# Optimization experiments

Hardware: AMD Instinct MI355X
Metric: run time of the kernel (lower is better)

## Reference

```python
import jax, jax.numpy as jnp
import numpy as np

B, N, Q, D = 1, 6, 10000, 256
HEADS, LEVELS, NPTS, ZANCH = 8, 1, 8, 4  # NPTS = 2*n_points, ZANCH = num_points_in_pillar
HF, WF = 32, 88
HD = D // HEADS


def setup_inputs() -> dict:
    key = jax.random.key(0)
    ks = jax.random.split(key, 18)
    s = 1.0 / np.sqrt(D)
    inp = {
        'queries': jax.random.normal(ks[0], (B, N, Q, D), jnp.float32),
        'pos_emb': jax.random.normal(ks[1], (B, N, Q, D), jnp.float32),
        'lvl_emb': jax.random.normal(ks[2], (LEVELS, D), jnp.float32),
        'cam_emb': jax.random.normal(ks[3], (N, D), jnp.float32),
        'features0': jax.random.normal(ks[4], (B * N, D, HF, WF), jnp.float32),
        'reference_points_3D': jax.random.uniform(ks[5], (B, N, Q, ZANCH, 2), jnp.float32),
        'bev_mask': jax.random.randint(ks[6], (B, N, Q, ZANCH, 2), 0, 2).astype(bool),
        # MSDeformAttn3D params
        'W_value': jax.random.normal(ks[7], (D, D), jnp.float32) * s,
        'b_value': jnp.zeros((D,), jnp.float32),
        'W_off': jax.random.normal(ks[8], (HEADS * LEVELS * NPTS * 2, D), jnp.float32) * 0.01,
        'b_off': jax.random.uniform(ks[9], (HEADS * LEVELS * NPTS * 2,), jnp.float32, -2.0, 2.0),
        'W_attn': jax.random.normal(ks[10], (HEADS * LEVELS * NPTS, D), jnp.float32) * s,
        'b_attn': jnp.zeros((HEADS * LEVELS * NPTS,), jnp.float32),
        'W_inner': jax.random.normal(ks[11], (D, D), jnp.float32) * s,
        'b_inner': jnp.zeros((D,), jnp.float32),
        # SpatialCrossAttention.output_proj
        'W_out': jax.random.normal(ks[12], (D, D), jnp.float32) * s,
        'b_out': jnp.zeros((D,), jnp.float32),
    }
    return inp


def _bilinear(value_t, loc, H, W):
    # value_t: (bn, heads, H*W, hd); loc: (bn, q, heads, pts, 2) normalized to [0,1]
    bn, q, heads, pts, _ = loc.shape
    hd = value_t.shape[-1]
    # grid_sample(2*loc-1, align_corners=False) -> pixel coord = loc*size - 0.5
    x = loc[..., 0] * W - 0.5
    y = loc[..., 1] * H - 0.5
    x0 = jnp.floor(x); y0 = jnp.floor(y)
    dx = x - x0; dy = y - y0
    x0 = x0.astype(jnp.int32); y0 = y0.astype(jnp.int32)
    out = jnp.zeros((bn, heads, q * pts, hd), value_t.dtype)
    corners = ((0, 0, (1 - dx) * (1 - dy)), (1, 0, dx * (1 - dy)),
               (0, 1, (1 - dx) * dy), (1, 1, dx * dy))
    for ox, oy, w in corners:
        xi = x0 + ox; yi = y0 + oy
        valid = (xi >= 0) & (xi < W) & (yi >= 0) & (yi < H)  # zero padding
        wgt = jnp.where(valid, w, 0.0)
        idx = jnp.clip(yi, 0, H - 1) * W + jnp.clip(xi, 0, W - 1)  # (bn,q,heads,pts)
        idx_t = idx.transpose(0, 2, 1, 3).reshape(bn, heads, q * pts)
        g = jnp.take_along_axis(value_t, idx_t[..., None], axis=2)  # (bn,heads,q*pts,hd)
        wgt_t = wgt.transpose(0, 2, 1, 3).reshape(bn, heads, q * pts)
        out = out + g * wgt_t[..., None]
    return out.reshape(bn, heads, q, pts, hd)


def _forward(queries, pos_emb, lvl_emb, cam_emb, features0, reference_points_3D, bev_mask,
             W_value, b_value, W_off, b_off, W_attn, b_attn, W_inner, b_inner, W_out, b_out):
    b, n, q, d = queries.shape
    hf, wf = features0.shape[-2:]
    # flatten features + level/cam embeddings -> (b*n, hw, d)
    feat = features0.reshape(b, n, d, hf * wf)
    feat = feat + lvl_emb[0][None, None, :, None] + cam_emb[None, :, :, None]
    input_flatten = feat.transpose(0, 1, 3, 2).reshape(b * n, hf * wf, d)

    qp = (queries + pos_emb).reshape(b * n, q, d)
    ref = reference_points_3D.reshape(b * n, q, ZANCH, 2)

    # --- MSDeformAttn3D (single level) ---
    value = (input_flatten @ W_value.T + b_value).reshape(b * n, hf * wf, HEADS, HD)
    off = (qp @ W_off.T + b_off).reshape(b * n, q, HEADS, LEVELS, NPTS, 2)
    attw = jax.nn.softmax((qp @ W_attn.T + b_attn).reshape(b * n, q, HEADS, LEVELS * NPTS), axis=-1)
    attw = attw.reshape(b * n, q, HEADS, LEVELS, NPTS)
    normalizer = jnp.array([wf, hf], queries.dtype)  # (W, H)
    pts_per_z = NPTS // ZANCH
    off_z = off.reshape(b * n, q, HEADS, LEVELS, pts_per_z, ZANCH, 2)
    loc = ref[:, :, None, None, None, :, :] + off_z / normalizer
    loc = loc.reshape(b * n, q, HEADS, LEVELS, NPTS, 2)

    value_t = value.transpose(0, 2, 1, 3)  # (bn, heads, hw, hd)
    sampled = _bilinear(value_t, loc[:, :, :, 0], hf, wf)  # (bn,heads,q,pts,hd)
    attw_t = attw[:, :, :, 0].transpose(0, 2, 1, 3)  # (bn,heads,q,pts)
    out = jnp.einsum('bhqp,bhqpc->bqhc', attw_t, sampled).reshape(b * n, q, d)
    out = out @ W_inner.T + b_inner

    # --- scatter back per camera, normalize by hit count ---
    attn = out.reshape(b, n, q, d)
    # indexes come from batch 0's mask (as in the original code)
    hit = (bev_mask[0, :, :, :, 0].astype(jnp.int32).sum(-1) > 0).astype(queries.dtype)  # (n,q)
    slots = (attn * hit[None, :, :, None]).sum(1)  # (b,q,d)
    count = (bev_mask[..., 0].astype(jnp.int32).sum(-1) > 0).astype(queries.dtype).sum(1)
    count = jnp.clip(count, 1.0, None)  # (b,q)
    slots = slots / count[..., None]
    return slots @ W_out.T + b_out


def reference(queries, pos_emb, lvl_emb, cam_emb, features0, reference_points_3D, bev_mask,
              W_value, b_value, W_off, b_off, W_attn, b_attn, W_inner, b_inner, W_out, b_out):
    return _forward(queries, pos_emb, lvl_emb, cam_emb, features0, reference_points_3D, bev_mask,
                    W_value, b_value, W_off, b_off, W_attn, b_attn, W_inner, b_inner, W_out, b_out)
```

## Files before the change

kernel.cpp:

```cpp
#include <hip/hip_runtime.h>
#include <hip/hip_bf16.h>

#define BN     6
#define NQ     10000
#define DIM    256
#define HEADS  8
#define HDD    32
#define HF_    32
#define WF_    88
#define HW_    (HF_*WF_)
#define MTOT   (BN*NQ)

typedef __attribute__((ext_vector_type(8))) unsigned short ushort8_t;
typedef __attribute__((ext_vector_type(8))) short bf16x8;
typedef __attribute__((ext_vector_type(4))) float f32x4;

static __device__ inline unsigned short f2bf(float x) {
    __hip_bfloat16 b = __float2bfloat16(x);
    return *(unsigned short*)&b;
}

__global__ __launch_bounds__(256)
void k_wcvt(const float* __restrict__ Wv, const float* __restrict__ Wo,
            const float* __restrict__ Wa, const float* __restrict__ Wi,
            const float* __restrict__ Wz,
            unsigned short* __restrict__ Wv_bf, unsigned short* __restrict__ Woa_bf,
            unsigned short* __restrict__ Wi_bf, unsigned short* __restrict__ Wz_bf)
{
    const int i4 = (blockIdx.x*256 + threadIdx.x) * 4;
    if (i4 < 65536) {
        float4 v;
        ushort4 p;
        v = *(const float4*)(Wv+i4); p.x=f2bf(v.x);p.y=f2bf(v.y);p.z=f2bf(v.z);p.w=f2bf(v.w);
        *(ushort4*)(Wv_bf+i4) = p;
        v = *(const float4*)(Wi+i4); p.x=f2bf(v.x);p.y=f2bf(v.y);p.z=f2bf(v.z);p.w=f2bf(v.w);
        *(ushort4*)(Wi_bf+i4) = p;
        v = *(const float4*)(Wz+i4); p.x=f2bf(v.x);p.y=f2bf(v.y);p.z=f2bf(v.z);p.w=f2bf(v.w);
        *(ushort4*)(Wz_bf+i4) = p;
    }
    if (i4 < 32768) {
        float4 v = *(const float4*)(Wo+i4);
        ushort4 p; p.x=f2bf(v.x);p.y=f2bf(v.y);p.z=f2bf(v.z);p.w=f2bf(v.w);
        *(ushort4*)(Woa_bf+i4) = p;
    }
    if (i4 < 16384) {
        float4 v = *(const float4*)(Wa+i4);
        ushort4 p; p.x=f2bf(v.x);p.y=f2bf(v.y);p.z=f2bf(v.z);p.w=f2bf(v.w);
        *(ushort4*)(Woa_bf+32768+i4) = p;
    }
}

__global__ __launch_bounds__(256)
void k_ebias(const float* __restrict__ lvl, const float* __restrict__ cam,
             const float* __restrict__ Wv, const float* __restrict__ bv,
             float* __restrict__ ebias)
{
    const int n = blockIdx.x;
    const int j = threadIdx.x;
    __shared__ float e[DIM];
    e[j] = lvl[j] + cam[n*DIM + j];
    __syncthreads();
    const float* w = Wv + (size_t)j*DIM;
    float s = bv[j];
    for (int d = 0; d < DIM; ++d) s += e[d]*w[d];
    ebias[n*DIM + j] = s;
}

__global__ __launch_bounds__(256)
void k_mask(const int* __restrict__ bev, float* __restrict__ hitf,
            float* __restrict__ scale, float* __restrict__ biasf)
{
    const int q = blockIdx.x*256 + threadIdx.x;
    if (q >= NQ) return;
    float cnt = 0.f;
    #pragma unroll
    for (int n = 0; n < BN; ++n) {
        int hit = 0;
        #pragma unroll
        for (int z = 0; z < 4; ++z)
            hit |= (bev[(((size_t)n*NQ + q)*4 + z)*2] != 0);
        hitf[(size_t)n*NQ + q] = (float)hit;
        cnt += (float)hit;
    }
    biasf[q] = (cnt > 0.f) ? 1.f : 0.f;
    scale[q] = 1.f / fmaxf(cnt, 1.f);
}

__global__ __launch_bounds__(256)
void k_feat(const float* __restrict__ feat, unsigned short* __restrict__ featT)
{
    __shared__ float Tf[64][68];
    const int cam = blockIdx.z;
    const int d0 = blockIdx.y * 64;
    const int p0 = blockIdx.x * 64;
    const int tid = threadIdx.x;
    #pragma unroll
    for (int i = 0; i < 4; ++i) {
        const int d = (tid>>4) + i*16;
        const int p4 = (tid&15)*4;
        *(float4*)&Tf[d][p4] = *(const float4*)(feat + ((size_t)cam*DIM + d0 + d)*HW_ + p0 + p4);
    }
    __syncthreads();
    const int p = tid>>2, dq = tid&3;
    unsigned short* ob = featT + ((size_t)cam*HW_ + p0 + p)*DIM + d0;
    #pragma unroll
    for (int i = 0; i < 4; ++i) {
        const int d4 = dq*4 + i*16;
        ushort4 pk;
        pk.x = f2bf(Tf[d4+0][p]); pk.y = f2bf(Tf[d4+1][p]);
        pk.z = f2bf(Tf[d4+2][p]); pk.w = f2bf(Tf[d4+3][p]);
        *(ushort4*)(ob + d4) = pk;
    }
}

__global__ __launch_bounds__(256)
void k_value_mfma(const unsigned short* __restrict__ featT,
                  const unsigned short* __restrict__ Wv_bf,
                  const float* __restrict__ ebias,
                  unsigned short* __restrict__ value_bf)
{
    __shared__ unsigned short Ap[128][72];
    __shared__ unsigned short Bc[64][72];
    const int cam = blockIdx.z;
    const int p0 = blockIdx.x * 128;
    const int c0 = blockIdx.y * 64;
    const int tid = threadIdx.x;
    const int lane = tid & 63, wave = tid >> 6;
    const int quad = lane >> 4, l15 = lane & 15;
    f32x4 acc[2][4] = {};
    const unsigned short* fbase = featT + ((size_t)cam*HW_ + p0)*DIM;

    for (int k0 = 0; k0 < DIM; k0 += 64) {
        #pragma unroll
        for (int i = 0; i < 4; ++i) {
            const int row = (tid>>3) + i*32;
            const int k8 = (tid&7)*8;
            *(ushort8_t*)&Ap[row][k8] = *(const ushort8_t*)(fbase + (size_t)row*DIM + k0 + k8);
        }
        #pragma unroll
        for (int i = 0; i < 2; ++i) {
            const int row = (tid>>3) + i*32;
            const int k8 = (tid&7)*8;
            *(ushort8_t*)&Bc[row][k8] = *(const ushort8_t*)(Wv_bf + (size_t)(c0+row)*DIM + k0 + k8);
        }
        __syncthreads();
        #pragma unroll
        for (int s = 0; s < 2; ++s) {
            const int kf = s*32 + quad*8;
            bf16x8 a[2], b[4];
            #pragma unroll
            for (int mt = 0; mt < 2; ++mt)
                a[mt] = *(const bf16x8*)&Ap[(wave*2+mt)*16 + l15][kf];
            #pragma unroll
            for (int nt = 0; nt < 4; ++nt)
                b[nt] = *(const bf16x8*)&Bc[nt*16 + l15][kf];
            #pragma unroll
            for (int mt = 0; mt < 2; ++mt)
                #pragma unroll
                for (int nt = 0; nt < 4; ++nt)
                    acc[mt][nt] = __builtin_amdgcn_mfma_f32_16x16x32_bf16(a[mt], b[nt], acc[mt][nt], 0,0,0);
        }
        __syncthreads();
    }
    #pragma unroll
    for (int nt = 0; nt < 4; ++nt) {
        const int c = c0 + nt*16 + l15;
        const float eb = ebias[cam*DIM + c];
        const int h = c >> 5, cc = c & 31;
        unsigned short* vb = value_bf + (size_t)(cam*HEADS + h)*HW_*HDD + cc;
        #pragma unroll
        for (int mt = 0; mt < 2; ++mt)
            #pragma unroll
            for (int r = 0; r < 4; ++r) {
                const int p = p0 + (wave*2+mt)*16 + quad*4 + r;
                vb[(size_t)p*HDD] = f2bf(acc[mt][nt][r] + eb);
            }
    }
}

__global__ __launch_bounds__(256)
void k_offattn(const float* __restrict__ Qr, const float* __restrict__ Pe,
               const unsigned short* __restrict__ Woa_bf,
               const float* __restrict__ boff, const float* __restrict__ battn,
               float* __restrict__ off_ws, float* __restrict__ attw_ws)
{
    const int tid = threadIdx.x;
    const int wave = tid >> 6, lane = tid & 63;
    const int quad = lane >> 4, l15 = lane & 15;
    const int m0 = (blockIdx.x*4 + wave) * 16;
    if (m0 >= MTOT) return;

    bf16x8 afr[8];
    {
        const float* qrow = Qr + (size_t)(m0 + l15)*DIM;
        const float* prow = Pe + (size_t)(m0 + l15)*DIM;
        #pragma unroll
        for (int kc = 0; kc < 8; ++kc) {
            const int k = kc*32 + quad*8;
            const float4 x0 = *(const float4*)(qrow + k);
            const float4 x1 = *(const float4*)(qrow + k + 4);
            const float4 y0 = *(const float4*)(prow + k);
            const float4 y1 = *(const float4*)(prow + k + 4);
            ushort8_t u;
            u[0]=f2bf(x0.x+y0.x); u[1]=f2bf(x0.y+y0.y); u[2]=f2bf(x0.z+y0.z); u[3]=f2bf(x0.w+y0.w);
            u[4]=f2bf(x1.x+y1.x); u[5]=f2bf(x1.y+y1.y); u[6]=f2bf(x1.z+y1.z); u[7]=f2bf(x1.w+y1.w);
            afr[kc] = *(bf16x8*)&u;
        }
    }

    f32x4 acc[12] = {};
    const unsigned short* bbase = Woa_bf + (size_t)l15*DIM + quad*8;
    #pragma unroll
    for (int kc = 0; kc < 8; ++kc) {
        bf16x8 b[12];
        #pragma unroll
        for (int nt = 0; nt < 12; ++nt)
            b[nt] = *(const bf16x8*)(bbase + (size_t)nt*16*DIM + kc*32);
        #pragma unroll
        for (int nt = 0; nt < 12; ++nt)
            acc[nt] = __builtin_amdgcn_mfma_f32_16x16x32_bf16(afr[kc], b[nt], acc[nt], 0,0,0);
    }

    #pragma unroll
    for (int nt = 0; nt < 12; ++nt) {
        const int col = nt*16 + l15;
        const float bias = (col < 128) ? boff[col] : battn[col-128];
        #pragma unroll
        for (int r = 0; r < 4; ++r) {
            const int m = m0 + quad*4 + r;
            const float v = acc[nt][r] + bias;
            if (col < 128) off_ws [(size_t)m*128 + col]      = v;
            else           attw_ws[(size_t)m*64 + (col-128)] = v;
        }
    }
}

__global__ __launch_bounds__(256)
void k_sample(const unsigned short* __restrict__ value_bf,
              const float* __restrict__ off_ws, const float* __restrict__ attw_ws,
              const float* __restrict__ ref3d, const float* __restrict__ hitf,
              const float* __restrict__ scale, unsigned short* __restrict__ asum_bf)
{
    const int gtid = blockIdx.x*256 + threadIdx.x;
    const int quarter = gtid & 3;
    const int h  = (gtid >> 2) & 7;
    const int q  = gtid >> 5;

    float acc[8];
    #pragma unroll
    for (int c = 0; c < 8; ++c) acc[c] = 0.f;

    #pragma unroll 1
    for (int n = 0; n < BN; ++n) {
        if (hitf[(size_t)n*NQ + q] == 0.f) continue;
        const size_t base = (size_t)n*NQ + q;

        const float4 a0 = *(const float4*)(attw_ws + base*64 + h*8);
        const float4 a1 = *(const float4*)(attw_ws + base*64 + h*8 + 4);
        float lg[8] = {a0.x,a0.y,a0.z,a0.w, a1.x,a1.y,a1.z,a1.w};
        float mx = -1e30f;
        #pragma unroll
        for (int p = 0; p < 8; ++p) mx = fmaxf(mx, lg[p]);
        float ssum = 0.f;
        #pragma unroll
        for (int p = 0; p < 8; ++p) { lg[p] = __expf(lg[p]-mx); ssum += lg[p]; }
        const float inv = 1.f/ssum;

        float off[16];
        #pragma unroll
        for (int i = 0; i < 4; ++i)
            *(float4*)&off[i*4] = *(const float4*)(off_ws + base*128 + h*16 + i*4);
        float ref[8];
        *(float4*)&ref[0] = *(const float4*)(ref3d + base*8);
        *(float4*)&ref[4] = *(const float4*)(ref3d + base*8 + 4);

        const unsigned short* vbase =
            value_bf + (size_t)(n*HEADS + h)*HW_*HDD + quarter*8;

        #pragma unroll
        for (int p = 0; p < 8; ++p) {
            const int z = p & 3;
            const float ax = ref[z*2+0]*WF_ + off[p*2+0] - 0.5f;
            const float ay = ref[z*2+1]*HF_ + off[p*2+1] - 0.5f;
            const float fx = floorf(ax), fy = floorf(ay);
            const float dx = ax-fx, dy = ay-fy;
            const int x0 = (int)fx, y0 = (int)fy;
            const float wp = lg[p]*inv;
            #pragma unroll
            for (int oy = 0; oy < 2; ++oy) {
                const int yi = y0 + oy;
                const float wy = oy ? dy : 1.f-dy;
                #pragma unroll
                for (int ox = 0; ox < 2; ++ox) {
                    const int xi = x0 + ox;
                    const float wx = ox ? dx : 1.f-dx;
                    const bool valid = ((unsigned)xi < WF_) & ((unsigned)yi < HF_);
                    const float cw = valid ? wp*wy*wx : 0.f;
                    const int xc = min(max(xi, 0), WF_-1);
                    const int yc = min(max(yi, 0), HF_-1);
                    const ushort8_t v = *(const ushort8_t*)(vbase + (size_t)(yc*WF_ + xc)*HDD);
                    #pragma unroll
                    for (int c = 0; c < 8; ++c)
                        acc[c] += cw * __uint_as_float(((unsigned)v[c]) << 16);
                }
            }
        }
    }

    const float sc = scale[q];
    ushort8_t o;
    #pragma unroll
    for (int c = 0; c < 8; ++c) o[c] = f2bf(acc[c]*sc);
    *(ushort8_t*)(asum_bf + (size_t)q*DIM + h*HDD + quarter*8) = o;
}

__global__ __launch_bounds__(256)
void k_gemm_mfma(const unsigned short* __restrict__ A_bf,
                 const unsigned short* __restrict__ W_bf,
                 const float* __restrict__ bias, const float* __restrict__ rowscale,
                 float* __restrict__ out_f, unsigned short* __restrict__ out_b, int M)
{
    __shared__ unsigned short As[128][72];
    __shared__ unsigned short Bs[64][72];
    const int m0 = blockIdx.x * 128;
    const int j0 = blockIdx.y * 64;
    const int tid = threadIdx.x;
    const int lane = tid & 63, wave = tid >> 6;
    const int quad = lane >> 4, l15 = lane & 15;
    f32x4 acc[2][4] = {};

    for (int k0 = 0; k0 < DIM; k0 += 64) {
        #pragma unroll
        for (int i = 0; i < 4; ++i) {
            const int row = (tid>>3) + i*32;
            const int k8 = (tid&7)*8;
            ushort8_t v = {0,0,0,0,0,0,0,0};
            if (m0 + row < M)
                v = *(const ushort8_t*)(A_bf + (size_t)(m0+row)*DIM + k0 + k8);
            *(ushort8_t*)&As[row][k8] = v;
        }
        #pragma unroll
        for (int i = 0; i < 2; ++i) {
            const int row = (tid>>3) + i*32;
            const int k8 = (tid&7)*8;
            *(ushort8_t*)&Bs[row][k8] = *(const ushort8_t*)(W_bf + (size_t)(j0+row)*DIM + k0 + k8);
        }
        __syncthreads();
        #pragma unroll
        for (int s = 0; s < 2; ++s) {
            const int kf = s*32 + quad*8;
            bf16x8 a[2], b[4];
            #pragma unroll
            for (int mt = 0; mt < 2; ++mt)
                a[mt] = *(const bf16x8*)&As[(wave*2+mt)*16 + l15][kf];
            #pragma unroll
            for (int nt = 0; nt < 4; ++nt)
                b[nt] = *(const bf16x8*)&Bs[nt*16 + l15][kf];
            #pragma unroll
            for (int mt = 0; mt < 2; ++mt)
                #pragma unroll
                for (int nt = 0; nt < 4; ++nt)
                    acc[mt][nt] = __builtin_amdgcn_mfma_f32_16x16x32_bf16(a[mt], b[nt], acc[mt][nt], 0,0,0);
        }
        __syncthreads();
    }
    #pragma unroll
    for (int nt = 0; nt < 4; ++nt) {
        const int j = j0 + nt*16 + l15;
        const float bj = bias[j];
        #pragma unroll
        for (int mt = 0; mt < 2; ++mt) {
            #pragma unroll
            for (int r = 0; r < 4; ++r) {
                const int m = m0 + (wave*2+mt)*16 + quad*4 + r;
                if (m >= M) continue;
                const float f = rowscale ? rowscale[m] : 1.f;
                const float v = acc[mt][nt][r] + f*bj;
                if (out_f) out_f[(size_t)m*DIM + j] = v;
                if (out_b) out_b[(size_t)m*DIM + j] = f2bf(v);
            }
        }
    }
}

extern "C" void kernel_launch(void* const* d_in, const int* in_sizes, int n_in,
                              void* d_out, int out_size, void* d_ws, size_t ws_size,
                              hipStream_t stream)
{
    const float* queries = (const float*)d_in[0];
    const float* pos_emb = (const float*)d_in[1];
    const float* lvl_emb = (const float*)d_in[2];
    const float* cam_emb = (const float*)d_in[3];
    const float* features= (const float*)d_in[4];
    const float* ref3d   = (const float*)d_in[5];
    const int*   bev     = (const int*)d_in[6];
    const float* Wv = (const float*)d_in[7];
    const float* bv = (const float*)d_in[8];
    const float* Wo = (const float*)d_in[9];
    const float* bo = (const float*)d_in[10];
    const float* Wa = (const float*)d_in[11];
    const float* ba = (const float*)d_in[12];
    const float* Wi = (const float*)d_in[13];
    const float* bi = (const float*)d_in[14];
    const float* Wz = (const float*)d_in[15];
    const float* bz = (const float*)d_in[16];
    float* out = (float*)d_out;

    char* ws = (char*)d_ws;
    size_t o = 0;
    auto alloc = [&](size_t bytes) { char* p = ws + o; o += (bytes + 255) & ~size_t(255); return p; };
    unsigned short* value_bf = (unsigned short*)alloc((size_t)BN*HEADS*HW_*HDD*2);
    unsigned short* featT    = (unsigned short*)alloc((size_t)BN*HW_*DIM*2);
    float* off_ws   = (float*)alloc((size_t)MTOT*128*4);
    float* attw_ws  = (float*)alloc((size_t)MTOT*64*4);
    unsigned short* asum_bf  = (unsigned short*)alloc((size_t)NQ*DIM*2);
    unsigned short* slots_bf = (unsigned short*)alloc((size_t)NQ*DIM*2);
    unsigned short* Wv_bf  = (unsigned short*)alloc(65536*2);
    unsigned short* Woa_bf = (unsigned short*)alloc(49152*2);
    unsigned short* Wi_bf  = (unsigned short*)alloc(65536*2);
    unsigned short* Wz_bf  = (unsigned short*)alloc(65536*2);
    float* hitf   = (float*)alloc((size_t)BN*NQ*4);
    float* scalev = (float*)alloc(NQ*4);
    float* biasf  = (float*)alloc(NQ*4);
    float* ebias  = (float*)alloc(BN*DIM*4);

    k_wcvt  <<<64, 256, 0, stream>>>(Wv, Wo, Wa, Wi, Wz, Wv_bf, Woa_bf, Wi_bf, Wz_bf);
    k_ebias <<<BN, 256, 0, stream>>>(lvl_emb, cam_emb, Wv, bv, ebias);
    k_mask  <<<(NQ+255)/256, 256, 0, stream>>>(bev, hitf, scalev, biasf);
    k_feat  <<<dim3(HW_/64, DIM/64, BN), 256, 0, stream>>>(features, featT);
    k_value_mfma<<<dim3(HW_/128, DIM/64, BN), 256, 0, stream>>>(featT, Wv_bf, ebias, value_bf);
    k_offattn<<<(MTOT/16 + 3)/4, 256, 0, stream>>>(queries, pos_emb, Woa_bf, bo, ba, off_ws, attw_ws);
    k_sample <<<NQ*32/256, 256, 0, stream>>>(value_bf, off_ws, attw_ws, ref3d, hitf, scalev, asum_bf);
    k_gemm_mfma<<<dim3((NQ+127)/128, DIM/64), 256, 0, stream>>>(asum_bf, Wi_bf, bi, biasf, nullptr, slots_bf, NQ);
    k_gemm_mfma<<<dim3((NQ+127)/128, DIM/64), 256, 0, stream>>>(slots_bf, Wz_bf, bz, nullptr, out, nullptr, NQ);
}
```

Baseline: 366.3 us.

## Fold inner and output projections into one GEMM, prefetch weights, batch sample loads

Precomputes the combined weight W_out·W_inner and its bias on device, replacing two back-to-back GEMMs with one and dropping the bf16 intermediate slots buffer. It also double-buffers the B-fragment loads in the offset/attention GEMM, adds occupancy hints to two kernels, and issues all four bilinear corner loads before accumulating in the sampler to raise memory-level parallelism. A small extra kernel computes the combined weight every call, and folding the weights in fp32 before bf16 rounding slightly changes the numerics.

```diff
diff --git a/kernel.cpp b/kernel.cpp
--- a/kernel.cpp
+++ b/kernel.cpp
@@ -22,21 +22,14 @@
 
 __global__ __launch_bounds__(256)
 void k_wcvt(const float* __restrict__ Wv, const float* __restrict__ Wo,
-            const float* __restrict__ Wa, const float* __restrict__ Wi,
-            const float* __restrict__ Wz,
-            unsigned short* __restrict__ Wv_bf, unsigned short* __restrict__ Woa_bf,
-            unsigned short* __restrict__ Wi_bf, unsigned short* __restrict__ Wz_bf)
+            const float* __restrict__ Wa,
+            unsigned short* __restrict__ Wv_bf, unsigned short* __restrict__ Woa_bf)
 {
     const int i4 = (blockIdx.x*256 + threadIdx.x) * 4;
     if (i4 < 65536) {
-        float4 v;
-        ushort4 p;
-        v = *(const float4*)(Wv+i4); p.x=f2bf(v.x);p.y=f2bf(v.y);p.z=f2bf(v.z);p.w=f2bf(v.w);
+        float4 v = *(const float4*)(Wv+i4);
+        ushort4 p; p.x=f2bf(v.x);p.y=f2bf(v.y);p.z=f2bf(v.z);p.w=f2bf(v.w);
         *(ushort4*)(Wv_bf+i4) = p;
-        v = *(const float4*)(Wi+i4); p.x=f2bf(v.x);p.y=f2bf(v.y);p.z=f2bf(v.z);p.w=f2bf(v.w);
-        *(ushort4*)(Wi_bf+i4) = p;
-        v = *(const float4*)(Wz+i4); p.x=f2bf(v.x);p.y=f2bf(v.y);p.z=f2bf(v.z);p.w=f2bf(v.w);
-        *(ushort4*)(Wz_bf+i4) = p;
     }
     if (i4 < 32768) {
         float4 v = *(const float4*)(Wo+i4);
@@ -47,6 +40,26 @@
         float4 v = *(const float4*)(Wa+i4);
         ushort4 p; p.x=f2bf(v.x);p.y=f2bf(v.y);p.z=f2bf(v.z);p.w=f2bf(v.w);
         *(ushort4*)(Woa_bf+32768+i4) = p;
+    }
+}
+
+__global__ __launch_bounds__(256)
+void k_wcomb(const float* __restrict__ Wz, const float* __restrict__ Wi,
+             const float* __restrict__ bi,
+             unsigned short* __restrict__ Wzi_bf, float* __restrict__ bzi)
+{
+    const int j = blockIdx.x;
+    const int k = threadIdx.x;
+    __shared__ float wzr[DIM];
+    wzr[k] = Wz[(size_t)j*DIM + k];
+    __syncthreads();
+    float s = 0.f;
+    for (int t = 0; t < DIM; ++t) s += wzr[t] * Wi[(size_t)t*DIM + k];
+    Wzi_bf[(size_t)j*DIM + k] = f2bf(s);
+    if (k == 0) {
+        float b = 0.f;
+        for (int t = 0; t < DIM; ++t) b += wzr[t] * bi[t];
+        bzi[j] = b;
     }
 }
 
@@ -178,7 +191,7 @@
     }
 }
 
-__global__ __launch_bounds__(256)
+__global__ __launch_bounds__(256, 2)
 void k_offattn(const float* __restrict__ Qr, const float* __restrict__ Pe,
                const unsigned short* __restrict__ Woa_bf,
                const float* __restrict__ boff, const float* __restrict__ battn,
@@ -210,15 +223,22 @@
 
     f32x4 acc[12] = {};
     const unsigned short* bbase = Woa_bf + (size_t)l15*DIM + quad*8;
+    bf16x8 bcur[12], bnxt[12];
+    #pragma unroll
+    for (int nt = 0; nt < 12; ++nt)
+        bcur[nt] = *(const bf16x8*)(bbase + (size_t)nt*16*DIM);
     #pragma unroll
     for (int kc = 0; kc < 8; ++kc) {
-        bf16x8 b[12];
+        if (kc < 7) {
+            #pragma unroll
+            for (int nt = 0; nt < 12; ++nt)
+                bnxt[nt] = *(const bf16x8*)(bbase + (size_t)nt*16*DIM + (kc+1)*32);
+        }
         #pragma unroll
         for (int nt = 0; nt < 12; ++nt)
-            b[nt] = *(const bf16x8*)(bbase + (size_t)nt*16*DIM + kc*32);
-        #pragma unroll
-        for (int nt = 0; nt < 12; ++nt)
-            acc[nt] = __builtin_amdgcn_mfma_f32_16x16x32_bf16(afr[kc], b[nt], acc[nt], 0,0,0);
+            acc[nt] = __builtin_amdgcn_mfma_f32_16x16x32_bf16(afr[kc], bcur[nt], acc[nt], 0,0,0);
+        #pragma unroll
+        for (int nt = 0; nt < 12; ++nt) bcur[nt] = bnxt[nt];
     }
 
     #pragma unroll
@@ -235,7 +255,7 @@
     }
 }
 
-__global__ __launch_bounds__(256)
+__global__ __launch_bounds__(256, 4)
 void k_sample(const unsigned short* __restrict__ value_bf,
               const float* __restrict__ off_ws, const float* __restrict__ attw_ws,
               const float* __restrict__ ref3d, const float* __restrict__ hitf,
@@ -286,24 +306,27 @@
             const float dx = ax-fx, dy = ay-fy;
             const int x0 = (int)fx, y0 = (int)fy;
             const float wp = lg[p]*inv;
-            #pragma unroll
-            for (int oy = 0; oy < 2; ++oy) {
-                const int yi = y0 + oy;
-                const float wy = oy ? dy : 1.f-dy;
+
+            int   cidx[4];
+            float cw[4];
+            #pragma unroll
+            for (int cc = 0; cc < 4; ++cc) {
+                const int oy = cc >> 1, ox = cc & 1;
+                const int yi = y0 + oy, xi = x0 + ox;
+                const float wgt = (oy ? dy : 1.f-dy) * (ox ? dx : 1.f-dx);
+                const bool valid = ((unsigned)xi < WF_) & ((unsigned)yi < HF_);
+                cw[cc]   = valid ? wp*wgt : 0.f;
+                cidx[cc] = min(max(yi,0), HF_-1)*WF_ + min(max(xi,0), WF_-1);
+            }
+            ushort8_t v[4];
+            #pragma unroll
+            for (int cc = 0; cc < 4; ++cc)
+                v[cc] = *(const ushort8_t*)(vbase + (size_t)cidx[cc]*HDD);
+            #pragma unroll
+            for (int cc = 0; cc < 4; ++cc)
                 #pragma unroll
-                for (int ox = 0; ox < 2; ++ox) {
-                    const int xi = x0 + ox;
-                    const float wx = ox ? dx : 1.f-dx;
-                    const bool valid = ((unsigned)xi < WF_) & ((unsigned)yi < HF_);
-                    const float cw = valid ? wp*wy*wx : 0.f;
-                    const int xc = min(max(xi, 0), WF_-1);
-                    const int yc = min(max(yi, 0), HF_-1);
-                    const ushort8_t v = *(const ushort8_t*)(vbase + (size_t)(yc*WF_ + xc)*HDD);
-                    #pragma unroll
-                    for (int c = 0; c < 8; ++c)
-                        acc[c] += cw * __uint_as_float(((unsigned)v[c]) << 16);
-                }
-            }
+                for (int c = 0; c < 8; ++c)
+                    acc[c] += cw[cc] * __uint_as_float(((unsigned)v[cc][c]) << 16);
         }
     }
 
@@ -317,8 +340,9 @@
 __global__ __launch_bounds__(256)
 void k_gemm_mfma(const unsigned short* __restrict__ A_bf,
                  const unsigned short* __restrict__ W_bf,
-                 const float* __restrict__ bias, const float* __restrict__ rowscale,
-                 float* __restrict__ out_f, unsigned short* __restrict__ out_b, int M)
+                 const float* __restrict__ b1, const float* __restrict__ rowscale,
+                 const float* __restrict__ b2,
+                 float* __restrict__ out_f, int M)
 {
     __shared__ unsigned short As[128][72];
     __shared__ unsigned short Bs[64][72];
@@ -367,17 +391,14 @@
     #pragma unroll
     for (int nt = 0; nt < 4; ++nt) {
         const int j = j0 + nt*16 + l15;
-        const float bj = bias[j];
+        const float b1j = b1[j], b2j = b2[j];
         #pragma unroll
         for (int mt = 0; mt < 2; ++mt) {
             #pragma unroll
             for (int r = 0; r < 4; ++r) {
                 const int m = m0 + (wave*2+mt)*16 + quad*4 + r;
                 if (m >= M) continue;
-                const float f = rowscale ? rowscale[m] : 1.f;
-                const float v = acc[mt][nt][r] + f*bj;
-                if (out_f) out_f[(size_t)m*DIM + j] = v;
-                if (out_b) out_b[(size_t)m*DIM + j] = f2bf(v);
+                out_f[(size_t)m*DIM + j] = acc[mt][nt][r] + rowscale[m]*b1j + b2j;
             }
         }
     }
@@ -414,23 +435,22 @@
     float* off_ws   = (float*)alloc((size_t)MTOT*128*4);
     float* attw_ws  = (float*)alloc((size_t)MTOT*64*4);
     unsigned short* asum_bf  = (unsigned short*)alloc((size_t)NQ*DIM*2);
-    unsigned short* slots_bf = (unsigned short*)alloc((size_t)NQ*DIM*2);
     unsigned short* Wv_bf  = (unsigned short*)alloc(65536*2);
     unsigned short* Woa_bf = (unsigned short*)alloc(49152*2);
-    unsigned short* Wi_bf  = (unsigned short*)alloc(65536*2);
-    unsigned short* Wz_bf  = (unsigned short*)alloc(65536*2);
+    unsigned short* Wzi_bf = (unsigned short*)alloc(65536*2);
+    float* bzi    = (float*)alloc(DIM*4);
     float* hitf   = (float*)alloc((size_t)BN*NQ*4);
     float* scalev = (float*)alloc(NQ*4);
     float* biasf  = (float*)alloc(NQ*4);
     float* ebias  = (float*)alloc(BN*DIM*4);
 
-    k_wcvt  <<<64, 256, 0, stream>>>(Wv, Wo, Wa, Wi, Wz, Wv_bf, Woa_bf, Wi_bf, Wz_bf);
+    k_wcvt  <<<64, 256, 0, stream>>>(Wv, Wo, Wa, Wv_bf, Woa_bf);
+    k_wcomb <<<DIM, 256, 0, stream>>>(Wz, Wi, bi, Wzi_bf, bzi);
     k_ebias <<<BN, 256, 0, stream>>>(lvl_emb, cam_emb, Wv, bv, ebias);
     k_mask  <<<(NQ+255)/256, 256, 0, stream>>>(bev, hitf, scalev, biasf);
     k_feat  <<<dim3(HW_/64, DIM/64, BN), 256, 0, stream>>>(features, featT);
     k_value_mfma<<<dim3(HW_/128, DIM/64, BN), 256, 0, stream>>>(featT, Wv_bf, ebias, value_bf);
     k_offattn<<<(MTOT/16 + 3)/4, 256, 0, stream>>>(queries, pos_emb, Woa_bf, bo, ba, off_ws, attw_ws);
     k_sample <<<NQ*32/256, 256, 0, stream>>>(value_bf, off_ws, attw_ws, ref3d, hitf, scalev, asum_bf);
-    k_gemm_mfma<<<dim3((NQ+127)/128, DIM/64), 256, 0, stream>>>(asum_bf, Wi_bf, bi, biasf, nullptr, slots_bf, NQ);
-    k_gemm_mfma<<<dim3((NQ+127)/128, DIM/64), 256, 0, stream>>>(slots_bf, Wz_bf, bz, nullptr, out, nullptr, NQ);
-}
+    k_gemm_mfma<<<dim3((NQ+127)/128, DIM/64), 256, 0, stream>>>(asum_bf, Wzi_bf, bzi, biasf, bz, out, NQ);
+}
```

After: 615.6 us. 1.68x slower.
